# Kernel optimization log

Measured on AMD Instinct MI355X. Metric: run time of the kernel, lower is better.

Reference implementation:

```python
import jax, jax.numpy as jnp
import numpy as np

IMPOSSIBLE = -10000.0  # DataConfig.IMPOSSIBLE_SCORE
B, L, V, E, H, T = 64, 512, 50000, 256, 512, 32


def setup_inputs() -> dict:
    key = jax.random.key(0)
    ks = jax.random.split(key, 15)
    s = 0.05
    return {
        "sents": jax.random.randint(ks[0], (B, L), 0, V),
        "lengths": jnp.full((B,), L, dtype=jnp.int32),
        "targets": jax.random.randint(ks[1], (B, L, T), 0, 2).astype(jnp.int32),
        "emb": jax.random.normal(ks[2], (V, E), jnp.float32) * s,
        "Wih_f": jax.random.normal(ks[3], (4 * H, E), jnp.float32) * s,
        "Whh_f": jax.random.normal(ks[4], (4 * H, H), jnp.float32) * s,
        "b_f": jax.random.normal(ks[5], (4 * H,), jnp.float32) * s,
        "Wih_b": jax.random.normal(ks[6], (4 * H, E), jnp.float32) * s,
        "Whh_b": jax.random.normal(ks[7], (4 * H, H), jnp.float32) * s,
        "b_b": jax.random.normal(ks[8], (4 * H,), jnp.float32) * s,
        "W_out": jax.random.normal(ks[9], (T, 2 * H), jnp.float32) * s,
        "b_out": jax.random.normal(ks[10], (T,), jnp.float32) * s,
        "start_trans": jax.random.normal(ks[11], (T,), jnp.float32),
        "end_trans": jax.random.normal(ks[12], (T,), jnp.float32),
        "trans": jnp.ones((T, T), jnp.float32) / T,
    }


def _lstm_dir(xW, Whh, reverse):
    # xW: (L, B, 4H) = x @ Wih.T + b, precomputed (the big GEMM, done once)
    h0 = jnp.zeros((xW.shape[1], Whh.shape[1]), xW.dtype)
    def step(carry, xw):
        h, c = carry
        g = xw + h @ Whh.T
        i, f, gg, o = jnp.split(g, 4, axis=-1)  # torch gate order i,f,g,o
        c = jax.nn.sigmoid(f) * c + jax.nn.sigmoid(i) * jnp.tanh(gg)
        h = jax.nn.sigmoid(o) * jnp.tanh(c)
        return (h, c), h
    _, hs = jax.lax.scan(step, (h0, h0), xW, reverse=reverse)
    return hs  # (L, B, H), in original time order


def _denominator(em, trans, start, end):
    # em: (L, B, T); CRF partition function via forward algorithm (mask = all ones)
    alpha0 = start + em[0]
    def step(alpha, e):
        inner = alpha[:, :, None] + trans[None] + e[:, None, :]  # (B, T, T)
        return jax.nn.logsumexp(inner, axis=1), None
    alpha, _ = jax.lax.scan(step, alpha0, em[1:])
    return jax.nn.logsumexp(alpha + end[None, :], axis=-1)  # (B,)


def _numerator(em, pt, trans, start, end):
    # em: (L, B, T); pt: (L, B, T) binary possible-tag mask (float)
    alpha0 = start + em[0]
    alpha0 = jnp.where(pt[0] == 0, IMPOSSIBLE, alpha0)
    def step(alpha, inputs):
        e, cur, nxt = inputs  # each (B, T)
        e = jnp.where(nxt == 0, IMPOSSIBLE, e)
        tr = jnp.where(cur[:, :, None] == 0, IMPOSSIBLE, trans[None])
        tr = jnp.where(nxt[:, None, :] == 0, IMPOSSIBLE, tr)
        inner = alpha[:, :, None] + e[:, None, :] + tr
        return jax.nn.logsumexp(inner, axis=1), None
    alpha, _ = jax.lax.scan(step, alpha0, (em[1:], pt[:-1], pt[1:]))
    et = end[None, :] * pt[-1]
    et = jnp.where(et == 0, IMPOSSIBLE, et)
    return jax.nn.logsumexp(alpha + et, axis=-1)  # (B,)


def reference(sents, lengths, targets, emb, Wih_f, Whh_f, b_f, Wih_b, Whh_b, b_b,
              W_out, b_out, start_trans, end_trans, trans):
    x = emb[sents]                      # (B, L, E)
    x = jnp.transpose(x, (1, 0, 2))     # (L, B, E) time-major
    hf = _lstm_dir(jnp.einsum('lbe,ge->lbg', x, Wih_f) + b_f, Whh_f, False)
    hb = _lstm_dir(jnp.einsum('lbe,ge->lbg', x, Wih_b) + b_b, Whh_b, True)
    em = jnp.einsum('lbh,th->lbt', jnp.concatenate([hf, hb], axis=-1), W_out) + b_out  # (L,B,T)
    pt = jnp.transpose(targets, (1, 0, 2)).astype(em.dtype)  # (L, B, T)
    gold = _numerator(em, pt, trans, start_trans, end_trans)
    fwd = _denominator(em, trans, start_trans, end_trans)
    return jnp.sum(fwd - gold)
```

## Files before the change

### kernel.cpp

```cpp
#include <hip/hip_runtime.h>


#define IMPOSSIBLE -10000.0f

typedef __attribute__((ext_vector_type(8))) short bf16x8;
typedef __attribute__((ext_vector_type(4))) float f32x4;
typedef unsigned int u32;
typedef unsigned short u16;

__device__ __forceinline__ u16 f2b(float f) {
  union { float f; u32 u; } v; v.f = f;
  return (u16)((v.u + 0x7fffu + ((v.u >> 16) & 1u)) >> 16);
}
__device__ __forceinline__ float sigm(float x) { return 1.0f / (1.0f + __expf(-x)); }
__device__ __forceinline__ float tanh_f(float x) { return 1.0f - 2.0f / (__expf(2.0f * x) + 1.0f); }

__global__ void k_init(u32* __restrict__ flg, float* __restrict__ out) {
  const int i = blockIdx.x * 256 + threadIdx.x;
  if (i < 4096)
    __hip_atomic_store(flg + i, 0u, __ATOMIC_RELAXED, __HIP_MEMORY_SCOPE_AGENT);
  if (i == 4096)
    __hip_atomic_store((u32*)out, 0u, __ATOMIC_RELAXED, __HIP_MEMORY_SCOPE_AGENT);
}

__global__ __launch_bounds__(256) void k_embed(
    const int* __restrict__ sents, const float* __restrict__ emb,
    u16* __restrict__ x2) {
  __shared__ int tok[64];
  const int tid = threadIdx.x, t = blockIdx.x;
  if (tid < 64) tok[tid] = sents[tid * 512 + t];
  __syncthreads();
#pragma unroll
  for (int i = 0; i < 16; ++i) {
    const int v = i * 256 + tid;
    const int row = v >> 6, ke = (v & 63) * 4;
    const float4 f = *(const float4*)(emb + (size_t)tok[row] * 256 + ke);
    ushort4 s; s.x = f2b(f.x); s.y = f2b(f.y); s.z = f2b(f.z); s.w = f2b(f.w);
    *(ushort4*)&x2[((size_t)t * 64 + row) * 256 + ke] = s;
  }
}

__global__ __launch_bounds__(256, 1) void k_lstm(
    const float* __restrict__ Whf, const float* __restrict__ Whb,
    const float* __restrict__ Wif, const float* __restrict__ Wib,
    const float* __restrict__ bf_, const float* __restrict__ bb_,
    const u16* __restrict__ x2, u16* __restrict__ H2, u32* __restrict__ flg) {
  __shared__ float pre4[4096];
  const int tid = threadIdx.x, wid = blockIdx.x;
  const int r = wid & 7, d = r >> 2, g = r & 3, s = wid >> 3;
  const int b0 = g * 16, j0 = s * 16;
  const float* __restrict__ Whh = d ? Whb : Whf;
  const float* __restrict__ Wih = d ? Wib : Wif;
  const float* __restrict__ bias = d ? bb_ : bf_;
  const int wv = tid >> 6, lane = tid & 63, lm = lane & 15, kh = lane >> 4;
  const int bl = tid >> 4, jj = tid & 15;

  bf16x8 wih_f[8], whh_f[16];
#pragma unroll
  for (int gg = 0; gg < 4; ++gg) {
    const float* wp = Wih + (size_t)(gg * 512 + j0 + lm) * 256 + wv * 64;
#pragma unroll
    for (int kt = 0; kt < 2; ++kt) {
      bf16x8 f;
#pragma unroll
      for (int j = 0; j < 8; ++j) f[j] = (short)f2b(wp[kt * 32 + kh * 8 + j]);
      wih_f[gg * 2 + kt] = f;
    }
    const float* wq = Whh + (size_t)(gg * 512 + j0 + lm) * 512 + wv * 128;
#pragma unroll
    for (int kt = 0; kt < 4; ++kt) {
      bf16x8 f;
#pragma unroll
      for (int j = 0; j < 8; ++j) f[j] = (short)f2b(wq[kt * 32 + kh * 8 + j]);
      whh_f[gg * 4 + kt] = f;
    }
  }
  const float b_i = bias[0 * 512 + j0 + jj];
  const float b_f = bias[1 * 512 + j0 + jj];
  const float b_g = bias[2 * 512 + j0 + jj];
  const float b_o = bias[3 * 512 + j0 + jj];

  u32* gflg = flg + (size_t)r * 512;
  float c = 0.f;
  const f32x4 z = {0.f, 0.f, 0.f, 0.f};
#pragma unroll 1
  for (int it = 0; it < 512; ++it) {
    const int tt = d ? (511 - it) : it;
    bf16x8 xa[2];
    {
      const u16* xp = x2 + ((size_t)tt * 64 + b0 + lm) * 256 + wv * 64 + kh * 8;
      xa[0] = *(const bf16x8*)xp;
      xa[1] = *(const bf16x8*)(xp + 32);
    }
    if (it > 0) {
      if (lane < 8) {
        const u32* fp = gflg + (wv * 8 + lane) * 16;
        int bud = 1 << 16;
        while (__hip_atomic_load(fp, __ATOMIC_RELAXED, __HIP_MEMORY_SCOPE_AGENT) <
                   (u32)it && --bud) {}
      }
      asm volatile("" ::: "memory");
    }
    f32x4 accg[4] = {z, z, z, z};
#pragma unroll
    for (int gg = 0; gg < 4; ++gg)
#pragma unroll
      for (int kt = 0; kt < 2; ++kt)
        accg[gg] = __builtin_amdgcn_mfma_f32_16x16x32_bf16(xa[kt], wih_f[gg * 2 + kt], accg[gg], 0, 0, 0);
    if (it > 0) {
      const int tp = d ? (tt + 1) : (tt - 1);
      bf16x8 ha[4];
#pragma unroll
      for (int kt = 0; kt < 4; ++kt) {
        const int sG = wv * 8 + kt * 2 + (kh >> 1);
        const u16* hp = H2 + ((((size_t)tp * 2 + d) * 4 + g) * 32 + sG) * 256 + lm * 16 + (kh & 1) * 8;
        ha[kt] = *(const bf16x8*)hp;
      }
#pragma unroll
      for (int gg = 0; gg < 4; ++gg)
#pragma unroll
        for (int kt = 0; kt < 4; ++kt)
          accg[gg] = __builtin_amdgcn_mfma_f32_16x16x32_bf16(ha[kt], whh_f[gg * 4 + kt], accg[gg], 0, 0, 0);
    }
#pragma unroll
    for (int gg = 0; gg < 4; ++gg)
      *(f32x4*)&pre4[wv * 1024 + gg * 256 + kh * 64 + lm * 4] = accg[gg];
    __syncthreads();
    const int off = (bl >> 2) * 64 + jj * 4 + (bl & 3);
    float pi = b_i, pf = b_f, pg = b_g, po = b_o;
#pragma unroll
    for (int w = 0; w < 4; ++w) {
      pi += pre4[w * 1024 + 0   + off];
      pf += pre4[w * 1024 + 256 + off];
      pg += pre4[w * 1024 + 512 + off];
      po += pre4[w * 1024 + 768 + off];
    }
    c = sigm(pf) * c + sigm(pi) * tanh_f(pg);
    const float h = sigm(po) * tanh_f(c);
    const float hq = __shfl_xor(h, 1);
    if ((tid & 1) == 0) {
      const u32 pk = (u32)f2b(h) | ((u32)f2b(hq) << 16);
      u32* hp2 = (u32*)H2 + ((((size_t)tt * 2 + d) * 4 + g) * 32 + s) * 128 + (tid >> 1);
      __hip_atomic_store(hp2, pk, __ATOMIC_RELAXED, __HIP_MEMORY_SCOPE_AGENT);
    }
    asm volatile("s_waitcnt vmcnt(0)" ::: "memory");
    __syncthreads();
    if (tid == 0)
      __hip_atomic_store(gflg + s * 16, (u32)(it + 1), __ATOMIC_RELAXED,
                         __HIP_MEMORY_SCOPE_AGENT);
  }
}

__global__ __launch_bounds__(256) void k_emproj(
    const u16* __restrict__ H2, const float* __restrict__ Wo,
    const float* __restrict__ bo, float* __restrict__ em) {
  __shared__ u16 Wl[32 * 1024];
  const int tid = threadIdx.x, mb = blockIdx.x;
  const int wv = tid >> 6, lane = tid & 63, lm = lane & 15, kh = lane >> 4;
#pragma unroll
  for (int i = 0; i < 32; ++i) {
    const int row = i, k = tid * 4;
    const float4 f = *(const float4*)(Wo + (size_t)row * 1024 + k);
    ushort4 s; s.x = f2b(f.x); s.y = f2b(f.y); s.z = f2b(f.z); s.w = f2b(f.w);
    *(ushort4*)&Wl[row * 1024 + ((k + 8 * row) & 1023)] = s;
  }
  __syncthreads();
  const f32x4 z = {0.f, 0.f, 0.f, 0.f};
  f32x4 acc[2] = {z, z};
#pragma unroll 2
  for (int kt = 0; kt < 32; ++kt) {
    const int dd = kt >> 4;
    const int sG = (kt & 15) * 2 + (kh >> 1);
    const u16* ap = H2 + ((((size_t)mb * 2 + dd) * 4 + wv) * 32 + sG) * 256 + lm * 16 + (kh & 1) * 8;
    const bf16x8 a = *(const bf16x8*)ap;
#pragma unroll
    for (int ni = 0; ni < 2; ++ni) {
      const int row = ni * 16 + lm;
      const bf16x8 b = *(const bf16x8*)&Wl[row * 1024 + ((kt * 32 + kh * 8 + 8 * row) & 1023)];
      acc[ni] = __builtin_amdgcn_mfma_f32_16x16x32_bf16(a, b, acc[ni], 0, 0, 0);
    }
  }
#pragma unroll
  for (int ni = 0; ni < 2; ++ni) {
    const int n = ni * 16 + lm;
    const float bv = bo[n];
#pragma unroll
    for (int rr = 0; rr < 4; ++rr) {
      const int m = mb * 64 + wv * 16 + kh * 4 + rr;
      em[(size_t)m * 32 + n] = acc[ni][rr] + bv;
    }
  }
}

__global__ __launch_bounds__(64) void k_crf(
    const float* __restrict__ em, const int* __restrict__ tgt,
    const float* __restrict__ trans, const float* __restrict__ stt,
    const float* __restrict__ ent, float* __restrict__ out) {
  __shared__ float trl[1024];
  __shared__ float al[32];
  __shared__ int cur[32];
  const int lane = threadIdx.x;
  const int b = blockIdx.x >> 1;
  const int isnum = blockIdx.x & 1;
#pragma unroll
  for (int i = 0; i < 16; ++i) trl[i * 64 + lane] = trans[i * 64 + lane];
  const int k = lane & 31, j0 = (lane >> 5) * 16;
  {
    float a0 = stt[k] + em[(size_t)b * 32 + k];
    int p0 = 1;
    if (isnum) { p0 = tgt[((size_t)b * 512) * 32 + k]; if (p0 == 0) a0 = IMPOSSIBLE; }
    if (lane < 32) { al[k] = a0; cur[k] = p0; }
  }
  __syncthreads();
  float emk = em[((size_t)64 + b) * 32 + k];
  int tg = isnum ? tgt[((size_t)b * 512 + 1) * 32 + k] : 1;
#pragma unroll 1
  for (int t = 1; t < 512; ++t) {
    const float e_raw = emk;
    const int nxt = tg;
    if (t + 1 < 512) {
      emk = em[((size_t)(t + 1) * 64 + b) * 32 + k];
      if (isnum) tg = tgt[((size_t)b * 512 + t + 1) * 32 + k];
    }
    const float e = (isnum && nxt == 0) ? IMPOSSIBLE : e_raw;
    float v[16];
    float m = -1e30f;
#pragma unroll
    for (int j = 0; j < 16; ++j) {
      float tr = trl[(j0 + j) * 32 + k];
      if (isnum && (cur[j0 + j] == 0 || nxt == 0)) tr = IMPOSSIBLE;
      v[j] = al[j0 + j] + tr;
      m = fmaxf(m, v[j]);
    }
    float ss = 0.f;
#pragma unroll
    for (int j = 0; j < 16; ++j) ss += __expf(v[j] - m);
    const float m2 = __shfl_xor(m, 32);
    const float s2 = __shfl_xor(ss, 32);
    const float M = fmaxf(m, m2);
    const float S = ss * __expf(m - M) + s2 * __expf(m2 - M);
    const float an = M + __logf(S) + e;
    __syncthreads();
    if (lane < 32) { al[k] = an; cur[k] = nxt; }
    __syncthreads();
  }
  float x;
  if (!isnum) {
    x = al[k] + ent[k];
  } else {
    const float et = ent[k] * (float)cur[k];
    x = al[k] + ((et == 0.f) ? IMPOSSIBLE : et);
  }
  float m = x;
#pragma unroll
  for (int o = 1; o < 32; o <<= 1) m = fmaxf(m, __shfl_xor(m, o));
  float ss = __expf(x - m);
#pragma unroll
  for (int o = 1; o < 32; o <<= 1) ss += __shfl_xor(ss, o);
  if (lane == 0) {
    const float rr = m + __logf(ss);
    atomicAdd(out, isnum ? -rr : rr);
  }
}

extern "C" void kernel_launch(void* const* d_in, const int* in_sizes, int n_in,
                              void* d_out, int out_size, void* d_ws, size_t ws_size,
                              hipStream_t stream) {
  (void)in_sizes; (void)n_in; (void)out_size; (void)ws_size;
  const int* sents = (const int*)d_in[0];
  const int* tgt = (const int*)d_in[2];
  const float* emb = (const float*)d_in[3];
  const float* Wif = (const float*)d_in[4];
  const float* Whf = (const float*)d_in[5];
  const float* bf_ = (const float*)d_in[6];
  const float* Wib = (const float*)d_in[7];
  const float* Whb = (const float*)d_in[8];
  const float* bb_ = (const float*)d_in[9];
  const float* Wo = (const float*)d_in[10];
  const float* bo = (const float*)d_in[11];
  const float* stt = (const float*)d_in[12];
  const float* ent = (const float*)d_in[13];
  const float* trans = (const float*)d_in[14];
  float* out = (float*)d_out;

  char* ws = (char*)d_ws;
  u16* x2 = (u16*)ws;
  u16* H2 = (u16*)(ws + 16777216ull);
  float* em = (float*)(ws + 83886080ull);
  u32* flg = (u32*)(ws + 88080384ull);

  k_init<<<dim3(17), dim3(256), 0, stream>>>(flg, out);
  k_embed<<<dim3(512), dim3(256), 0, stream>>>(sents, emb, x2);
  k_lstm<<<dim3(256), dim3(256), 0, stream>>>(Whf, Whb, Wif, Wib, bf_, bb_, x2, H2, flg);
  k_emproj<<<dim3(512), dim3(256), 0, stream>>>(H2, Wo, bo, em);
  k_crf<<<dim3(128), dim3(64), 0, stream>>>(em, tgt, trans, stt, ent, out);
}
```

Before: 1.827 ms.

## Replace LSTM flag barriers with parity bits embedded in hidden-state data

Removes the separate per-block step flags and the vmcnt drain before signalling. The parity of the step is now stored in the low mantissa bit of each bf16 hidden value, and a pre-fill kernel initialises H2 with the opposite parity. Consumers poll the hidden values themselves and use them directly once all parity bits match, which takes the flag round-trip off the recurrence's critical path. In exchange it truncates one mantissa bit of h, adds a fill pass over H2, and relies on 64-bit relaxed loads and 32-bit stores each being seen whole.

```diff
diff --git a/kernel.cpp b/kernel.cpp
--- a/kernel.cpp
+++ b/kernel.cpp
@@ -7,6 +7,7 @@
 typedef __attribute__((ext_vector_type(4))) float f32x4;
 typedef unsigned int u32;
 typedef unsigned short u16;
+typedef unsigned long long u64;
 
 __device__ __forceinline__ u16 f2b(float f) {
   union { float f; u32 u; } v; v.f = f;
@@ -15,12 +16,19 @@
 __device__ __forceinline__ float sigm(float x) { return 1.0f / (1.0f + __expf(-x)); }
 __device__ __forceinline__ float tanh_f(float x) { return 1.0f - 2.0f / (__expf(2.0f * x) + 1.0f); }
 
-__global__ void k_init(u32* __restrict__ flg, float* __restrict__ out) {
-  const int i = blockIdx.x * 256 + threadIdx.x;
-  if (i < 4096)
-    __hip_atomic_store(flg + i, 0u, __ATOMIC_RELAXED, __HIP_MEMORY_SCOPE_AGENT);
-  if (i == 4096)
+__global__ void k_init(float* __restrict__ out) {
+  if (threadIdx.x == 0)
     __hip_atomic_store((u32*)out, 0u, __ATOMIC_RELAXED, __HIP_MEMORY_SCOPE_AGENT);
+}
+
+__global__ __launch_bounds__(256) void k_fill(u64* __restrict__ H2q) {
+  const size_t i0 = ((size_t)blockIdx.x * 256 + threadIdx.x) * 4;
+  const int t = (int)(i0 >> 14);
+  const int d = (int)((i0 >> 13) & 1);
+  const u64 val = ((t + d + 1) & 1) ? 0x0001000100010001ull : 0ull;
+#pragma unroll
+  for (int k = 0; k < 4; ++k)
+    __hip_atomic_store(H2q + i0 + k, val, __ATOMIC_RELAXED, __HIP_MEMORY_SCOPE_AGENT);
 }
 
 __global__ __launch_bounds__(256) void k_embed(
@@ -44,7 +52,7 @@
     const float* __restrict__ Whf, const float* __restrict__ Whb,
     const float* __restrict__ Wif, const float* __restrict__ Wib,
     const float* __restrict__ bf_, const float* __restrict__ bb_,
-    const u16* __restrict__ x2, u16* __restrict__ H2, u32* __restrict__ flg) {
+    const u16* __restrict__ x2, u16* __restrict__ H2) {
   __shared__ float pre4[4096];
   const int tid = threadIdx.x, wid = blockIdx.x;
   const int r = wid & 7, d = r >> 2, g = r & 3, s = wid >> 3;
@@ -80,27 +88,33 @@
   const float b_g = bias[2 * 512 + j0 + jj];
   const float b_o = bias[3 * 512 + j0 + jj];
 
-  u32* gflg = flg + (size_t)r * 512;
+  const u64 PM = 0x0001000100010001ull;
   float c = 0.f;
   const f32x4 z = {0.f, 0.f, 0.f, 0.f};
 #pragma unroll 1
   for (int it = 0; it < 512; ++it) {
     const int tt = d ? (511 - it) : it;
+    u64 hv[8];
+    const u64* hb8[8];
+    if (it > 0) {
+      const int tp = d ? (tt + 1) : (tt - 1);
+#pragma unroll
+      for (int kt = 0; kt < 4; ++kt) {
+        const int sG = wv * 8 + kt * 2 + (kh >> 1);
+        const u64* base = (const u64*)H2 +
+            ((((size_t)tp * 2 + d) * 4 + g) * 32 + sG) * 64 + lm * 4 + (kh & 1) * 2;
+        hb8[kt * 2] = base; hb8[kt * 2 + 1] = base + 1;
+      }
+#pragma unroll
+      for (int i = 0; i < 8; ++i)
+        hv[i] = __hip_atomic_load(hb8[i], __ATOMIC_RELAXED, __HIP_MEMORY_SCOPE_AGENT);
+    }
     bf16x8 xa[2];
     {
       const u16* xp = x2 + ((size_t)tt * 64 + b0 + lm) * 256 + wv * 64 + kh * 8;
       xa[0] = *(const bf16x8*)xp;
       xa[1] = *(const bf16x8*)(xp + 32);
     }
-    if (it > 0) {
-      if (lane < 8) {
-        const u32* fp = gflg + (wv * 8 + lane) * 16;
-        int bud = 1 << 16;
-        while (__hip_atomic_load(fp, __ATOMIC_RELAXED, __HIP_MEMORY_SCOPE_AGENT) <
-                   (u32)it && --bud) {}
-      }
-      asm volatile("" ::: "memory");
-    }
     f32x4 accg[4] = {z, z, z, z};
 #pragma unroll
     for (int gg = 0; gg < 4; ++gg)
@@ -108,13 +122,25 @@
       for (int kt = 0; kt < 2; ++kt)
         accg[gg] = __builtin_amdgcn_mfma_f32_16x16x32_bf16(xa[kt], wih_f[gg * 2 + kt], accg[gg], 0, 0, 0);
     if (it > 0) {
-      const int tp = d ? (tt + 1) : (tt - 1);
+      const u64 want = ((it - 1) & 1) ? PM : 0ull;
+      bool ok = true;
+#pragma unroll
+      for (int i = 0; i < 8; ++i) ok &= ((hv[i] & PM) == want);
+      int bud = 1 << 13;
+      while (!ok && --bud) {
+#pragma unroll
+        for (int i = 0; i < 8; ++i)
+          hv[i] = __hip_atomic_load(hb8[i], __ATOMIC_RELAXED, __HIP_MEMORY_SCOPE_AGENT);
+        ok = true;
+#pragma unroll
+        for (int i = 0; i < 8; ++i) ok &= ((hv[i] & PM) == want);
+      }
       bf16x8 ha[4];
 #pragma unroll
       for (int kt = 0; kt < 4; ++kt) {
-        const int sG = wv * 8 + kt * 2 + (kh >> 1);
-        const u16* hp = H2 + ((((size_t)tp * 2 + d) * 4 + g) * 32 + sG) * 256 + lm * 16 + (kh & 1) * 8;
-        ha[kt] = *(const bf16x8*)hp;
+        union { u64 q[2]; bf16x8 v; } cv;
+        cv.q[0] = hv[kt * 2]; cv.q[1] = hv[kt * 2 + 1];
+        ha[kt] = cv.v;
       }
 #pragma unroll
       for (int gg = 0; gg < 4; ++gg)
@@ -139,15 +165,14 @@
     const float h = sigm(po) * tanh_f(c);
     const float hq = __shfl_xor(h, 1);
     if ((tid & 1) == 0) {
-      const u32 pk = (u32)f2b(h) | ((u32)f2b(hq) << 16);
+      const u32 p = (u32)(it & 1);
+      const u32 lo = ((u32)f2b(h) & 0xFFFEu) | p;
+      const u32 hi = ((u32)f2b(hq) & 0xFFFEu) | p;
+      const u32 pk = lo | (hi << 16);
       u32* hp2 = (u32*)H2 + ((((size_t)tt * 2 + d) * 4 + g) * 32 + s) * 128 + (tid >> 1);
       __hip_atomic_store(hp2, pk, __ATOMIC_RELAXED, __HIP_MEMORY_SCOPE_AGENT);
     }
-    asm volatile("s_waitcnt vmcnt(0)" ::: "memory");
     __syncthreads();
-    if (tid == 0)
-      __hip_atomic_store(gflg + s * 16, (u32)(it + 1), __ATOMIC_RELAXED,
-                         __HIP_MEMORY_SCOPE_AGENT);
   }
 }
 
@@ -287,11 +312,11 @@
   u16* x2 = (u16*)ws;
   u16* H2 = (u16*)(ws + 16777216ull);
   float* em = (float*)(ws + 83886080ull);
-  u32* flg = (u32*)(ws + 88080384ull);
-
-  k_init<<<dim3(17), dim3(256), 0, stream>>>(flg, out);
+
+  k_init<<<dim3(1), dim3(64), 0, stream>>>(out);
+  k_fill<<<dim3(8192), dim3(256), 0, stream>>>((u64*)H2);
   k_embed<<<dim3(512), dim3(256), 0, stream>>>(sents, emb, x2);
-  k_lstm<<<dim3(256), dim3(256), 0, stream>>>(Whf, Whb, Wif, Wib, bf_, bb_, x2, H2, flg);
+  k_lstm<<<dim3(256), dim3(256), 0, stream>>>(Whf, Whb, Wif, Wib, bf_, bb_, x2, H2);
   k_emproj<<<dim3(512), dim3(256), 0, stream>>>(H2, Wo, bo, em);
   k_crf<<<dim3(128), dim3(64), 0, stream>>>(em, tgt, trans, stt, ent, out);
 }
```

Result: slower. 1.939 ms (+6.1%).
